# Optimization experiments

Hardware: AMD Instinct MI355X
Metric: run time of the kernel (lower is better)

## Reference

```python
import jax, jax.numpy as jnp
import numpy as np

N_NODES = 50000
N_EDGES = 200000
N_GRAPHS = 2048
EMB = 300
N_LAYERS = 5
BN_EPS = 1e-5


def setup_inputs() -> dict:
    key = jax.random.key(0)
    ks = jax.random.split(key, 16)
    s = 0.02
    d = {}
    d["atomic_number"] = jax.random.randint(ks[0], (N_NODES,), 0, 120)
    d["chirality_type"] = jax.random.randint(ks[1], (N_NODES,), 0, 3)
    d["bond_type"] = jax.random.randint(ks[2], (N_EDGES,), 0, 6)
    d["bond_direction_type"] = jax.random.randint(ks[3], (N_EDGES,), 0, 3)
    d["src"] = jax.random.randint(ks[4], (N_EDGES,), 0, N_NODES)
    d["dst"] = jax.random.randint(ks[5], (N_EDGES,), 0, N_NODES)
    d["graph_ids"] = jnp.sort(jax.random.randint(ks[6], (N_NODES,), 0, N_GRAPHS))
    d["num_graphs"] = N_GRAPHS
    d["node_emb0"] = jax.random.normal(ks[7], (120, EMB), jnp.float32) * s
    d["node_emb1"] = jax.random.normal(ks[8], (3, EMB), jnp.float32) * s
    d["edge_emb0"] = jax.random.normal(ks[9], (N_LAYERS, 6, EMB), jnp.float32) * s
    d["edge_emb1"] = jax.random.normal(ks[10], (N_LAYERS, 3, EMB), jnp.float32) * s
    d["W1"] = jax.random.normal(ks[11], (N_LAYERS, EMB, 2 * EMB), jnp.float32) * s
    d["b1"] = jnp.zeros((N_LAYERS, 2 * EMB), jnp.float32)
    d["W2"] = jax.random.normal(ks[12], (N_LAYERS, 2 * EMB, EMB), jnp.float32) * s
    d["b2"] = jnp.zeros((N_LAYERS, EMB), jnp.float32)
    d["bn_gamma"] = jnp.ones((N_LAYERS, EMB), jnp.float32)
    d["bn_beta"] = jnp.zeros((N_LAYERS, EMB), jnp.float32)
    d["bn_mean"] = jax.random.normal(ks[13], (N_LAYERS, EMB), jnp.float32) * s
    d["bn_var"] = jax.random.uniform(ks[14], (N_LAYERS, EMB), jnp.float32, 0.5, 1.5)
    return d


def gin_node_feats(atomic_number, chirality_type, bond_type, bond_direction_type,
                   src, dst, node_emb0, node_emb1, edge_emb0, edge_emb1,
                   W1, b1, W2, b2, bn_gamma, bn_beta, bn_mean, bn_var):
    n = atomic_number.shape[0]
    h = node_emb0[atomic_number] + node_emb1[chirality_type]  # [N, EMB]
    feats = [h]
    for l in range(N_LAYERS):
        # u_add_e message: src node feat + per-layer categorical edge embedding
        e = edge_emb0[l][bond_type] + edge_emb1[l][bond_direction_type]  # [E, EMB]
        m = feats[l][src] + e
        agg = jax.ops.segment_sum(m, dst, num_segments=n)  # sum aggregation at dst
        x = jax.nn.relu(agg @ W1[l] + b1[l]) @ W2[l] + b2[l]  # GIN MLP 300->600->300
        # BatchNorm1d in eval mode (running stats)
        x = (x - bn_mean[l]) * jax.lax.rsqrt(bn_var[l] + BN_EPS) * bn_gamma[l] + bn_beta[l]
        if l < N_LAYERS - 1:
            x = jax.nn.relu(x)  # activation on all but last layer
        feats.append(x)  # dropout is identity in eval mode
    return jnp.concatenate(feats, axis=1)  # JK='concat' -> [N, 6*EMB]


def reference(atomic_number, chirality_type, bond_type, bond_direction_type,
              src, dst, graph_ids, num_graphs,
              node_emb0, node_emb1, edge_emb0, edge_emb1,
              W1, b1, W2, b2, bn_gamma, bn_beta, bn_mean, bn_var):
    nf = gin_node_feats(atomic_number, chirality_type, bond_type, bond_direction_type,
                        src, dst, node_emb0, node_emb1, edge_emb0, edge_emb1,
                        W1, b1, W2, b2, bn_gamma, bn_beta, bn_mean, bn_var)
    sums = jax.ops.segment_sum(nf, graph_ids, num_segments=num_graphs)  # SumPooling
    counts = jax.ops.segment_sum(jnp.ones((nf.shape[0], 1), nf.dtype), graph_ids,
                                 num_segments=num_graphs)
    avg = sums / jnp.maximum(counts, 1.0)  # AvgPooling
    return jnp.concatenate([avg, sums], axis=1)  # [G, 2*6*EMB]
```

## Files before the change

kernel.cpp:

```cpp
#include <hip/hip_runtime.h>

#define EMB 300
#define HID 600
#define NL 5
#define BN_EPS 1e-5f

#define FS 320
#define HS 640
#define NPW 8
#define KS1 10
#define KS2 20

typedef __attribute__((ext_vector_type(8))) short short8;
typedef __attribute__((ext_vector_type(4))) float f32x4;
typedef __attribute__((ext_vector_type(4))) unsigned short us4;

__device__ __forceinline__ unsigned short f2bf(float x) {
    unsigned u = __float_as_uint(x);
    unsigned r = (u + 0x7FFFu + ((u >> 16) & 1u)) >> 16;
    return (unsigned short)r;
}
__device__ __forceinline__ float bf2f(unsigned short h) {
    return __uint_as_float(((unsigned)h) << 16);
}

#define GLDS16(gsrc, ldst)                                                     \
    __builtin_amdgcn_global_load_lds(                                          \
        (const __attribute__((address_space(1))) unsigned int*)(gsrc),         \
        (__attribute__((address_space(3))) unsigned int*)(ldst), 16, 0, 0)

__global__ void k_init_h0(const int* __restrict__ an, const int* __restrict__ ch,
                          const float* __restrict__ ne0, const float* __restrict__ ne1,
                          unsigned short* __restrict__ Fb, int n) {
    int t = blockIdx.x * blockDim.x + threadIdx.x;
    int i = t / (FS / 4), f4 = t - i * (FS / 4);
    if (i >= n) return;
    int f = f4 * 4;
    us4 h = {0, 0, 0, 0};
    if (f < EMB) {
        const float4 a = *(const float4*)(ne0 + (size_t)an[i] * EMB + f);
        const float4 b = *(const float4*)(ne1 + (size_t)ch[i] * EMB + f);
        h[0] = f2bf(a.x + b.x); h[1] = f2bf(a.y + b.y);
        h[2] = f2bf(a.z + b.z); h[3] = f2bf(a.w + b.w);
    }
    *(us4*)(Fb + (size_t)i * FS + f) = h;
}

__global__ void k_hist(const int* __restrict__ dst, const int* __restrict__ bt,
                       const int* __restrict__ bd, int* __restrict__ deg,
                       int* __restrict__ cnt9, int e) {
    int t = blockIdx.x * blockDim.x + threadIdx.x;
    if (t >= e) return;
    int d = dst[t];
    atomicAdd(&deg[d], 1);
    atomicAdd(&cnt9[d * 9 + bt[t]], 1);
    atomicAdd(&cnt9[d * 9 + 6 + bd[t]], 1);
}

__global__ __launch_bounds__(256)
void k_scan_blk(const int* __restrict__ deg, int* __restrict__ incl,
                int* __restrict__ part, int n) {
    int tid = threadIdx.x;
    int base = blockIdx.x * 1024 + tid * 4;
    int v0 = (base + 0 < n) ? deg[base + 0] : 0;
    int v1 = (base + 1 < n) ? deg[base + 1] : 0;
    int v2 = (base + 2 < n) ? deg[base + 2] : 0;
    int v3 = (base + 3 < n) ? deg[base + 3] : 0;
    int ts = v0 + v1 + v2 + v3;
    int lane = tid & 63, w = tid >> 6;
    int x = ts;
#pragma unroll
    for (int off = 1; off < 64; off <<= 1) {
        int y = __shfl_up(x, off);
        if (lane >= off) x += y;
    }
    __shared__ int ws[4];
    if (lane == 63) ws[w] = x;
    __syncthreads();
    int woff = 0;
    for (int i = 0; i < w; ++i) woff += ws[i];
    int r = woff + x - ts;
    r += v0; if (base + 0 < n) incl[base + 0] = r;
    r += v1; if (base + 1 < n) incl[base + 1] = r;
    r += v2; if (base + 2 < n) incl[base + 2] = r;
    r += v3; if (base + 3 < n) incl[base + 3] = r;
    if (tid == 255) part[blockIdx.x] = woff + x;
}

__global__ __launch_bounds__(1024)
void k_scan_part(int* __restrict__ part, int nb) {
    int tid = threadIdx.x;
    int v = (tid < nb) ? part[tid] : 0;
    int lane = tid & 63, w = tid >> 6;
    int x = v;
#pragma unroll
    for (int off = 1; off < 64; off <<= 1) {
        int y = __shfl_up(x, off);
        if (lane >= off) x += y;
    }
    __shared__ int ws[16];
    if (lane == 63) ws[w] = x;
    __syncthreads();
    int woff = 0;
    for (int i = 0; i < w; ++i) woff += ws[i];
    if (tid < nb) part[tid] = woff + x - v;
}

__global__ void k_scan_add(const int* __restrict__ incl, const int* __restrict__ part,
                           const int* __restrict__ deg, int* __restrict__ roff,
                           int* __restrict__ curs, int n) {
    int i = blockIdx.x * blockDim.x + threadIdx.x;
    if (i >= n) return;
    int inc = incl[i] + part[i >> 10];
    roff[i + 1] = inc;
    curs[i] = inc - deg[i];
    if (i == 0) roff[0] = 0;
}

__global__ void k_scatter(const int* __restrict__ dst, const int* __restrict__ src,
                          int* __restrict__ cursor, int* __restrict__ srcs, int e) {
    int t = blockIdx.x * blockDim.x + threadIdx.x;
    if (t < e) { int p = atomicAdd(&cursor[dst[t]], 1); srcs[p] = src[t]; }
}

__global__ void k_gbound(const int* __restrict__ gids, int* __restrict__ gstart,
                         int n, int G) {
    int i = blockIdx.x * blockDim.x + threadIdx.x;
    if (i >= n) return;
    int g = gids[i];
    int gp = (i == 0) ? -1 : gids[i - 1];
    for (int q = gp + 1; q <= g; ++q) gstart[q] = i;
    if (i == n - 1)
        for (int q = g + 1; q <= G; ++q) gstart[q] = n;
}

__global__ void k_prep_w1p(const float* __restrict__ W1, unsigned short* __restrict__ W1P,
                           int total) {
    int t = blockIdx.x * blockDim.x + threadIdx.x;
    if (t >= total) return;
    int lane = t & 63;
    int r = t >> 6;
    int ks = r % KS1; r /= KS1;
    int nf = r % 40;
    int l = r / 40;
    int n = nf * 16 + (lane & 15);
    int kb = ks * 32 + (lane >> 4) * 8;
    unsigned short v[8];
#pragma unroll
    for (int e = 0; e < 8; ++e) {
        int k = kb + e;
        v[e] = (n < HID && k < EMB) ? f2bf(W1[(size_t)l * EMB * HID + (size_t)k * HID + n]) : 0;
    }
    *(short8*)(W1P + (size_t)t * 8) = *(short8*)v;
}

__global__ void k_prep_w2p(const float* __restrict__ W2, unsigned short* __restrict__ W2P,
                           int total) {
    int t = blockIdx.x * blockDim.x + threadIdx.x;
    if (t >= total) return;
    int lane = t & 63;
    int r = t >> 6;
    int ks = r % KS2; r /= KS2;
    int nf = r % 20;
    int l = r / 20;
    int n = nf * 16 + (lane & 15);
    int kb = ks * 32 + (lane >> 4) * 8;
    unsigned short v[8];
#pragma unroll
    for (int e = 0; e < 8; ++e) {
        int k = kb + e;
        v[e] = (n < EMB && k < HID) ? f2bf(W2[(size_t)l * HID * EMB + (size_t)k * EMB + n]) : 0;
    }
    *(short8*)(W2P + (size_t)t * 8) = *(short8*)v;
}

__global__ void k_prep_params(const float* __restrict__ b1, const float* __restrict__ b2,
                              const float* __restrict__ g, const float* __restrict__ be,
                              const float* __restrict__ mu, const float* __restrict__ va,
                              float* __restrict__ b1p, float* __restrict__ scp,
                              float* __restrict__ shp, int total) {
    int t = blockIdx.x * blockDim.x + threadIdx.x;
    if (t >= total) return;
    int n = t % HS, l = t / HS;
    b1p[t] = (n < HID) ? b1[l * HID + n] : 0.f;
    if (n < FS) {
        float sc = 0.f, sh = 0.f;
        if (n < EMB) {
            sc = g[l * EMB + n] * rsqrtf(va[l * EMB + n] + BN_EPS);
            sh = be[l * EMB + n] + (b2[l * EMB + n] - mu[l * EMB + n]) * sc;
        }
        scp[l * FS + n] = sc;
        shp[l * FS + n] = sh;
    }
}

__global__ __launch_bounds__(256)
void k_aggregate(const unsigned short* __restrict__ fb,
                 const float* __restrict__ e0, const float* __restrict__ e1,
                 const int* __restrict__ roff, const int* __restrict__ srcs,
                 const int* __restrict__ cnt9,
                 unsigned short* __restrict__ agg, int n) {
    const int v0 = (blockIdx.x * 4 + (threadIdx.x >> 6)) * NPW;
    if (v0 >= n) return;
    const int lane = threadIdx.x & 63;
    const int nv = min(NPW, n - v0);

    int rv = 0;
    {
        int idx = v0 + lane;
        if (lane <= NPW && idx <= n) rv = roff[idx];
    }
    const int base = __shfl(rv, 0);
    const int total = __shfl(rv, nv) - base;

    const int n9 = n * 9;
    const int base9 = v0 * 9;
    int c0 = (base9 + lane < n9) ? cnt9[base9 + lane] : 0;
    int c1 = (lane < 8 && base9 + 64 + lane < n9) ? cnt9[base9 + 64 + lane] : 0;

    int c = 0;
    int chunk = 0;
    auto nextIdx = [&]() -> int {
        if ((c & 63) == 0)
            chunk = (c + lane < total) ? srcs[base + c + lane] : 0;
        int r = __shfl(chunk, c & 63);
        ++c;
        return r;
    };

#pragma unroll
    for (int i = 0; i < NPW; ++i) {
        if (i < nv) {
            const int di = __shfl(rv, i + 1) - __shfl(rv, i);
            float aA[4] = {0.f, 0.f, 0.f, 0.f};
            float aB[4] = {0.f, 0.f, 0.f, 0.f};
            int k = 0;
            for (; k + 4 <= di; k += 4) {
                int i0 = nextIdx(), i1 = nextIdx(), i2 = nextIdx(), i3 = nextIdx();
                const us4* r0 = (const us4*)(fb + (size_t)i0 * FS);
                const us4* r1 = (const us4*)(fb + (size_t)i1 * FS);
                const us4* r2 = (const us4*)(fb + (size_t)i2 * FS);
                const us4* r3 = (const us4*)(fb + (size_t)i3 * FS);
                us4 x0 = r0[lane], x1 = r1[lane], x2 = r2[lane], x3 = r3[lane];
                us4 y0 = {}, y1 = {}, y2 = {}, y3 = {};
                if (lane < 11) { y0 = r0[64 + lane]; y1 = r1[64 + lane];
                                 y2 = r2[64 + lane]; y3 = r3[64 + lane]; }
#pragma unroll
                for (int q = 0; q < 4; ++q)
                    aA[q] += (bf2f(x0[q]) + bf2f(x1[q])) + (bf2f(x2[q]) + bf2f(x3[q]));
                if (lane < 11) {
#pragma unroll
                    for (int q = 0; q < 4; ++q)
                        aB[q] += (bf2f(y0[q]) + bf2f(y1[q])) + (bf2f(y2[q]) + bf2f(y3[q]));
                }
            }
            for (; k < di; ++k) {
                int i0 = nextIdx();
                const us4* r0 = (const us4*)(fb + (size_t)i0 * FS);
                us4 x0 = r0[lane];
#pragma unroll
                for (int q = 0; q < 4; ++q) aA[q] += bf2f(x0[q]);
                if (lane < 11) {
                    us4 y0 = r0[64 + lane];
#pragma unroll
                    for (int q = 0; q < 4; ++q) aB[q] += bf2f(y0[q]);
                }
            }
#pragma unroll
            for (int t = 0; t < 9; ++t) {
                const int pos = i * 9 + t;
                int cv = __shfl(pos < 64 ? c0 : c1, pos & 63);
                if (cv) {
                    float fc = (float)cv;
                    const float* row = (t < 6) ? (e0 + t * EMB) : (e1 + (t - 6) * EMB);
                    f32x4 ea = *(const f32x4*)(row + 4 * lane);
#pragma unroll
                    for (int q = 0; q < 4; ++q) aA[q] += fc * ea[q];
                    if (lane < 11) {
                        f32x4 eb = *(const f32x4*)(row + 256 + 4 * lane);
#pragma unroll
                        for (int q = 0; q < 4; ++q) aB[q] += fc * eb[q];
                    }
                }
            }
            us4* ar = (us4*)(agg + (size_t)(v0 + i) * FS);
            us4 h;
#pragma unroll
            for (int q = 0; q < 4; ++q) h[q] = f2bf(aA[q]);
            ar[lane] = h;
            if (lane < 11) {
                us4 hb;
#pragma unroll
                for (int q = 0; q < 4; ++q) hb[q] = f2bf(aB[q]);
                ar[64 + lane] = hb;
            }
        }
    }
}

template <int EPI>
__global__ __launch_bounds__(512)
void k_mlp(const unsigned short* __restrict__ A,
           const unsigned short* __restrict__ W1P,
           const unsigned short* __restrict__ W2P,
           const float* __restrict__ b1p,
           const float* __restrict__ scp, const float* __restrict__ shp,
           unsigned short* __restrict__ Cout) {
    __shared__ unsigned short Ash[64 * 320];
    __shared__ unsigned short Hsh[64 * 640];
    const int tid = threadIdx.x;
    const int lane = tid & 63, wid = tid >> 6;
    const int lr = lane & 15, lk = lane >> 4, rgrp = lk * 4;
    const size_t m0s = (size_t)blockIdx.x * 64;

#pragma unroll
    for (int cch = 0; cch < 5; ++cch) {
        const int sbase = wid * 5120 + cch * 1024;
        const int s = sbase + lane * 16;
        const int row = s / 640;
        const int u = s ^ ((row & 7) << 4);
        GLDS16((const char*)A + m0s * 640 + u, (char*)Ash + sbase);
    }
    asm volatile("s_waitcnt vmcnt(0)" ::: "memory");
    __syncthreads();

    {
        f32x4 acc1[5][4] = {};
        short8 bw[5], bn_[5];
#pragma unroll
        for (int i = 0; i < 5; ++i)
            bw[i] = *(const short8*)(W1P + (((size_t)(wid * 5 + i) * KS1 + 0) * 64 + lane) * 8);
        for (int ks = 0; ks < KS1; ++ks) {
            if (ks + 1 < KS1) {
#pragma unroll
                for (int i = 0; i < 5; ++i)
                    bn_[i] = *(const short8*)(W1P + (((size_t)(wid * 5 + i) * KS1 + ks + 1) * 64 + lane) * 8);
            }
            short8 a[4];
#pragma unroll
            for (int j = 0; j < 4; ++j) {
                const int row = j * 16 + lr;
                const int o = (row * 640 + ks * 64 + lk * 16) ^ ((lr & 7) << 4);
                a[j] = *(const short8*)((const char*)Ash + o);
            }
#pragma unroll
            for (int i = 0; i < 5; ++i)
#pragma unroll
                for (int j = 0; j < 4; ++j)
                    acc1[i][j] = __builtin_amdgcn_mfma_f32_16x16x32_bf16(bw[i], a[j], acc1[i][j], 0, 0, 0);
#pragma unroll
            for (int i = 0; i < 5; ++i) bw[i] = bn_[i];
        }
#pragma unroll
        for (int i = 0; i < 5; ++i) {
            const int n0 = wid * 80 + i * 16 + rgrp;
            const f32x4 q0 = *(const f32x4*)&b1p[n0];
#pragma unroll
            for (int j = 0; j < 4; ++j) {
                const int m = j * 16 + lr;
                us4 h;
#pragma unroll
                for (int p = 0; p < 4; ++p)
                    h[p] = f2bf(fmaxf(acc1[i][j][p] + q0[p], 0.f));
                const int o = (m * 1280 + n0 * 2) ^ ((lr & 7) << 4);
                *(us4*)((char*)Hsh + o) = h;
            }
        }
    }
    __syncthreads();

    {
        const int wm2 = wid >> 2, wn2 = wid & 3;
        f32x4 acc2[5][2] = {};
        short8 cw[5], cn_[5];
#pragma unroll
        for (int i = 0; i < 5; ++i)
            cw[i] = *(const short8*)(W2P + (((size_t)(wn2 * 5 + i) * KS2 + 0) * 64 + lane) * 8);
        for (int ks = 0; ks < KS2; ++ks) {
            if (ks + 1 < KS2) {
#pragma unroll
                for (int i = 0; i < 5; ++i)
                    cn_[i] = *(const short8*)(W2P + (((size_t)(wn2 * 5 + i) * KS2 + ks + 1) * 64 + lane) * 8);
            }
            short8 a[2];
#pragma unroll
            for (int j = 0; j < 2; ++j) {
                const int row = wm2 * 32 + j * 16 + lr;
                const int o = (row * 1280 + ks * 64 + lk * 16) ^ ((lr & 7) << 4);
                a[j] = *(const short8*)((const char*)Hsh + o);
            }
#pragma unroll
            for (int i = 0; i < 5; ++i)
#pragma unroll
                for (int j = 0; j < 2; ++j)
                    acc2[i][j] = __builtin_amdgcn_mfma_f32_16x16x32_bf16(cw[i], a[j], acc2[i][j], 0, 0, 0);
#pragma unroll
            for (int i = 0; i < 5; ++i) cw[i] = cn_[i];
        }
#pragma unroll
        for (int i = 0; i < 5; ++i) {
            const int n0 = wn2 * 80 + i * 16 + rgrp;
            const f32x4 q0 = *(const f32x4*)&scp[n0];
            const f32x4 q1 = *(const f32x4*)&shp[n0];
#pragma unroll
            for (int j = 0; j < 2; ++j) {
                const size_t m = m0s + (size_t)(wm2 * 32 + j * 16 + lr);
                us4 h;
#pragma unroll
                for (int p = 0; p < 4; ++p) {
                    float x = acc2[i][j][p] * q0[p] + q1[p];
                    if (EPI == 1) x = fmaxf(x, 0.f);
                    h[p] = f2bf(x);
                }
                *(us4*)(Cout + m * FS + n0) = h;
            }
        }
    }
}

__global__ __launch_bounds__(256)
void k_pool(const unsigned short* __restrict__ feats, const int* __restrict__ gstart,
            float* __restrict__ out, int l) {
    const int g = blockIdx.x;
    const int tid = threadIdx.x;
    const int w = tid >> 6, lane = tid & 63;
    const int s = gstart[g], e = gstart[g + 1];
    float aA[4] = {0.f, 0.f, 0.f, 0.f};
    float aB[4] = {0.f, 0.f, 0.f, 0.f};
    int v = s + w;
    for (; v + 4 < e; v += 8) {
        const us4* r0 = (const us4*)(feats + (size_t)v * FS);
        const us4* r1 = (const us4*)(feats + (size_t)(v + 4) * FS);
        us4 x0 = r0[lane], x1 = r1[lane];
        us4 y0 = {}, y1 = {};
        if (lane < 11) { y0 = r0[64 + lane]; y1 = r1[64 + lane]; }
#pragma unroll
        for (int q = 0; q < 4; ++q) aA[q] += bf2f(x0[q]) + bf2f(x1[q]);
        if (lane < 11) {
#pragma unroll
            for (int q = 0; q < 4; ++q) aB[q] += bf2f(y0[q]) + bf2f(y1[q]);
        }
    }
    if (v < e) {
        const us4* r0 = (const us4*)(feats + (size_t)v * FS);
        us4 x0 = r0[lane];
#pragma unroll
        for (int q = 0; q < 4; ++q) aA[q] += bf2f(x0[q]);
        if (lane < 11) {
            us4 y0 = r0[64 + lane];
#pragma unroll
            for (int q = 0; q < 4; ++q) aB[q] += bf2f(y0[q]);
        }
    }
    __shared__ f32x4 smA[4][64];
    __shared__ f32x4 smB[4][16];
    f32x4 xa;
#pragma unroll
    for (int q = 0; q < 4; ++q) xa[q] = aA[q];
    smA[w][lane] = xa;
    if (lane < 16) {
        f32x4 xb;
#pragma unroll
        for (int q = 0; q < 4; ++q) xb[q] = aB[q];
        smB[w][lane] = xb;
    }
    __syncthreads();
    if (w == 0) {
        f32x4 t = smA[0][lane] + smA[1][lane] + smA[2][lane] + smA[3][lane];
        float inv = 1.0f / fmaxf((float)(e - s), 1.0f);
        float* oavg = out + (size_t)g * (12 * EMB) + l * EMB;
        float* osum = oavg + 6 * EMB;
        *(f32x4*)(oavg + 4 * lane) = t * inv;
        *(f32x4*)(osum + 4 * lane) = t;
        if (lane < 11) {
            f32x4 tb = smB[0][lane] + smB[1][lane] + smB[2][lane] + smB[3][lane];
            *(f32x4*)(oavg + 256 + 4 * lane) = tb * inv;
            *(f32x4*)(osum + 256 + 4 * lane) = tb;
        }
    }
}

extern "C" void kernel_launch(void* const* d_in, const int* in_sizes, int n_in,
                              void* d_out, int out_size, void* d_ws, size_t ws_size,
                              hipStream_t stream) {
    const int*   an  = (const int*)d_in[0];
    const int*   ch  = (const int*)d_in[1];
    const int*   bt  = (const int*)d_in[2];
    const int*   bd  = (const int*)d_in[3];
    const int*   src = (const int*)d_in[4];
    const int*   dst = (const int*)d_in[5];
    const int*   gid = (const int*)d_in[6];
    const float* ne0 = (const float*)d_in[8];
    const float* ne1 = (const float*)d_in[9];
    const float* ee0 = (const float*)d_in[10];
    const float* ee1 = (const float*)d_in[11];
    const float* W1  = (const float*)d_in[12];
    const float* b1  = (const float*)d_in[13];
    const float* W2  = (const float*)d_in[14];
    const float* b2  = (const float*)d_in[15];
    const float* bng = (const float*)d_in[16];
    const float* bnb = (const float*)d_in[17];
    const float* bnm = (const float*)d_in[18];
    const float* bnv = (const float*)d_in[19];

    const int N = in_sizes[0];
    const int E = in_sizes[2];
    const int G = out_size / (12 * EMB);
    const int M_pad = ((N + 63) / 64) * 64;
    const int MT = M_pad / 64;
    const int nb = (N + 1023) / 1024;

    char* ws = (char*)d_ws;
    size_t off = 0;
    auto alloc = [&](size_t bytes) -> void* {
        void* p = (void*)(ws + off);
        off += (bytes + 255) & ~(size_t)255;
        return p;
    };
    unsigned short* Fb0  = (unsigned short*)alloc((size_t)M_pad * FS * 2);
    unsigned short* Fb1  = (unsigned short*)alloc((size_t)M_pad * FS * 2);
    unsigned short* A1   = (unsigned short*)alloc((size_t)M_pad * FS * 2);
    unsigned short* W1P  = (unsigned short*)alloc((size_t)NL * 40 * KS1 * 64 * 8 * 2);
    unsigned short* W2P  = (unsigned short*)alloc((size_t)NL * 20 * KS2 * 64 * 8 * 2);
    float*          b1p  = (float*)alloc((size_t)NL * HS * 4);
    float*          scp  = (float*)alloc((size_t)NL * FS * 4);
    float*          shp  = (float*)alloc((size_t)NL * FS * 4);
    int*            deg  = (int*)alloc((size_t)N * 4);
    int*            roff = (int*)alloc(((size_t)N + 1) * 4);
    int*            curs = (int*)alloc((size_t)N * 4);
    int*            srcs = (int*)alloc((size_t)E * 4);
    int*            cnt9 = (int*)alloc((size_t)N * 9 * 4);
    int*            incl = (int*)alloc((size_t)N * 4);
    int*            part = (int*)alloc((size_t)1024 * 4);
    int*            gst  = (int*)alloc(((size_t)G + 1) * 4);

    {
        int t1 = NL * 40 * KS1 * 64;
        k_prep_w1p<<<(t1 + 255) / 256, 256, 0, stream>>>(W1, W1P, t1);
        int t2 = NL * 20 * KS2 * 64;
        k_prep_w2p<<<(t2 + 255) / 256, 256, 0, stream>>>(W2, W2P, t2);
        int t3 = NL * HS;
        k_prep_params<<<(t3 + 255) / 256, 256, 0, stream>>>(b1, b2, bng, bnb, bnm, bnv,
                                                            b1p, scp, shp, t3);
    }

    {
        int tt = N * (FS / 4);
        k_init_h0<<<(tt + 255) / 256, 256, 0, stream>>>(an, ch, ne0, ne1, Fb0, N);
    }

    hipMemsetAsync(deg, 0, (size_t)N * 4, stream);
    hipMemsetAsync(cnt9, 0, (size_t)N * 9 * 4, stream);
    k_hist<<<(E + 255) / 256, 256, 0, stream>>>(dst, bt, bd, deg, cnt9, E);
    k_scan_blk<<<nb, 256, 0, stream>>>(deg, incl, part, N);
    k_scan_part<<<1, 1024, 0, stream>>>(part, nb);
    k_scan_add<<<(N + 255) / 256, 256, 0, stream>>>(incl, part, deg, roff, curs, N);
    k_scatter<<<(E + 255) / 256, 256, 0, stream>>>(dst, src, curs, srcs, E);
    k_gbound<<<(N + 255) / 256, 256, 0, stream>>>(gid, gst, N, G);

    const int aggBlocks = (N + 4 * NPW - 1) / (4 * NPW);

    unsigned short* Fbc = Fb0;
    unsigned short* Fbo = Fb1;
    for (int l = 0; l < NL; ++l) {
        k_pool<<<G, 256, 0, stream>>>(Fbc, gst, (float*)d_out, l);
        k_aggregate<<<aggBlocks, 256, 0, stream>>>(Fbc,
                                                   ee0 + (size_t)l * 6 * EMB,
                                                   ee1 + (size_t)l * 3 * EMB,
                                                   roff, srcs, cnt9, A1, N);
        const unsigned short* W1Pl = W1P + (size_t)l * 40 * KS1 * 64 * 8;
        const unsigned short* W2Pl = W2P + (size_t)l * 20 * KS2 * 64 * 8;
        if (l < NL - 1)
            k_mlp<1><<<MT, 512, 0, stream>>>(A1, W1Pl, W2Pl,
                                             b1p + (size_t)l * HS,
                                             scp + (size_t)l * FS, shp + (size_t)l * FS,
                                             Fbo);
        else
            k_mlp<2><<<MT, 512, 0, stream>>>(A1, W1Pl, W2Pl,
                                             b1p + (size_t)l * HS,
                                             scp + (size_t)l * FS, shp + (size_t)l * FS,
                                             Fbo);
        unsigned short* t = Fbc; Fbc = Fbo; Fbo = t;
    }
    k_pool<<<G, 256, 0, stream>>>(Fbc, gst, (float*)d_out, NL);
}
```

Baseline: 755.3 us.

## Load MLP inputs directly from global, drop A staging in LDS, retile GEMM1

The fused MLP kernel no longer stages the 64-row input tile in LDS through global_load_lds. Each wave now reads its A fragments straight from global memory, and GEMM1 is retiled into 2x4 waves over two column halves. The weight prefetch double-buffering is removed, MFMA blocks are wrapped in s_setprio, and launch bounds request 4 blocks per CU. Cutting LDS use is meant to raise occupancy and drop a barrier, in exchange for redundant global loads of A across waves and no explicit latency hiding for weight loads.

```diff
diff --git a/kernel.cpp b/kernel.cpp
--- a/kernel.cpp
+++ b/kernel.cpp
@@ -23,11 +23,6 @@
 __device__ __forceinline__ float bf2f(unsigned short h) {
     return __uint_as_float(((unsigned)h) << 16);
 }
-
-#define GLDS16(gsrc, ldst)                                                     \
-    __builtin_amdgcn_global_load_lds(                                          \
-        (const __attribute__((address_space(1))) unsigned int*)(gsrc),         \
-        (__attribute__((address_space(3))) unsigned int*)(ldst), 16, 0, 0)
 
 __global__ void k_init_h0(const int* __restrict__ an, const int* __restrict__ ch,
                           const float* __restrict__ ne0, const float* __restrict__ ne1,
@@ -299,120 +294,109 @@
 }
 
 template <int EPI>
-__global__ __launch_bounds__(512)
+__global__ __launch_bounds__(512, 4)
 void k_mlp(const unsigned short* __restrict__ A,
            const unsigned short* __restrict__ W1P,
            const unsigned short* __restrict__ W2P,
            const float* __restrict__ b1p,
            const float* __restrict__ scp, const float* __restrict__ shp,
            unsigned short* __restrict__ Cout) {
-    __shared__ unsigned short Ash[64 * 320];
     __shared__ unsigned short Hsh[64 * 640];
     const int tid = threadIdx.x;
     const int lane = tid & 63, wid = tid >> 6;
+    const int wm = wid >> 2, wn = wid & 3;
     const int lr = lane & 15, lk = lane >> 4, rgrp = lk * 4;
-    const size_t m0s = (size_t)blockIdx.x * 64;
-
-#pragma unroll
-    for (int cch = 0; cch < 5; ++cch) {
-        const int sbase = wid * 5120 + cch * 1024;
-        const int s = sbase + lane * 16;
-        const int row = s / 640;
-        const int u = s ^ ((row & 7) << 4);
-        GLDS16((const char*)A + m0s * 640 + u, (char*)Ash + sbase);
-    }
-    asm volatile("s_waitcnt vmcnt(0)" ::: "memory");
+    const size_t m0 = (size_t)blockIdx.x * 64;
+
+    const unsigned short* a0p = A + (m0 + (size_t)(wm * 32 + lr)) * FS + lk * 8;
+    const unsigned short* a1p = a0p + (size_t)16 * FS;
+
+#pragma unroll
+    for (int h = 0; h < 2; ++h) {
+        f32x4 acc1[5][2] = {};
+        const unsigned short* wp = W1P + ((size_t)(h * 20 + wn * 5) * KS1 * 64 + lane) * 8;
+        for (int ks = 0; ks < KS1; ++ks) {
+            short8 a0 = *(const short8*)(a0p + ks * 32);
+            short8 a1 = *(const short8*)(a1p + ks * 32);
+            short8 w0 = *(const short8*)(wp + ((size_t)(0 * KS1 + ks) * 64) * 8);
+            short8 w1 = *(const short8*)(wp + ((size_t)(1 * KS1 + ks) * 64) * 8);
+            short8 w2 = *(const short8*)(wp + ((size_t)(2 * KS1 + ks) * 64) * 8);
+            short8 w3 = *(const short8*)(wp + ((size_t)(3 * KS1 + ks) * 64) * 8);
+            short8 w4 = *(const short8*)(wp + ((size_t)(4 * KS1 + ks) * 64) * 8);
+            __builtin_amdgcn_s_setprio(1);
+            acc1[0][0] = __builtin_amdgcn_mfma_f32_16x16x32_bf16(w0, a0, acc1[0][0], 0, 0, 0);
+            acc1[0][1] = __builtin_amdgcn_mfma_f32_16x16x32_bf16(w0, a1, acc1[0][1], 0, 0, 0);
+            acc1[1][0] = __builtin_amdgcn_mfma_f32_16x16x32_bf16(w1, a0, acc1[1][0], 0, 0, 0);
+            acc1[1][1] = __builtin_amdgcn_mfma_f32_16x16x32_bf16(w1, a1, acc1[1][1], 0, 0, 0);
+            acc1[2][0] = __builtin_amdgcn_mfma_f32_16x16x32_bf16(w2, a0, acc1[2][0], 0, 0, 0);
+            acc1[2][1] = __builtin_amdgcn_mfma_f32_16x16x32_bf16(w2, a1, acc1[2][1], 0, 0, 0);
+            acc1[3][0] = __builtin_amdgcn_mfma_f32_16x16x32_bf16(w3, a0, acc1[3][0], 0, 0, 0);
+            acc1[3][1] = __builtin_amdgcn_mfma_f32_16x16x32_bf16(w3, a1, acc1[3][1], 0, 0, 0);
+            acc1[4][0] = __builtin_amdgcn_mfma_f32_16x16x32_bf16(w4, a0, acc1[4][0], 0, 0, 0);
+            acc1[4][1] = __builtin_amdgcn_mfma_f32_16x16x32_bf16(w4, a1, acc1[4][1], 0, 0, 0);
+            __builtin_amdgcn_s_setprio(0);
+        }
+#pragma unroll
+        for (int i = 0; i < 5; ++i) {
+            const int n0 = h * 320 + wn * 80 + i * 16 + rgrp;
+            const f32x4 q0 = *(const f32x4*)&b1p[n0];
+#pragma unroll
+            for (int j = 0; j < 2; ++j) {
+                const int m = wm * 32 + j * 16 + lr;
+                us4 hh;
+#pragma unroll
+                for (int p = 0; p < 4; ++p)
+                    hh[p] = f2bf(fmaxf(acc1[i][j][p] + q0[p], 0.f));
+                const int o = (m * 1280 + n0 * 2) ^ ((lr & 7) << 4);
+                *(us4*)((char*)Hsh + o) = hh;
+            }
+        }
+    }
     __syncthreads();
 
     {
-        f32x4 acc1[5][4] = {};
-        short8 bw[5], bn_[5];
-#pragma unroll
-        for (int i = 0; i < 5; ++i)
-            bw[i] = *(const short8*)(W1P + (((size_t)(wid * 5 + i) * KS1 + 0) * 64 + lane) * 8);
-        for (int ks = 0; ks < KS1; ++ks) {
-            if (ks + 1 < KS1) {
-#pragma unroll
-                for (int i = 0; i < 5; ++i)
-                    bn_[i] = *(const short8*)(W1P + (((size_t)(wid * 5 + i) * KS1 + ks + 1) * 64 + lane) * 8);
-            }
-            short8 a[4];
-#pragma unroll
-            for (int j = 0; j < 4; ++j) {
-                const int row = j * 16 + lr;
-                const int o = (row * 640 + ks * 64 + lk * 16) ^ ((lr & 7) << 4);
-                a[j] = *(const short8*)((const char*)Ash + o);
-            }
-#pragma unroll
-            for (int i = 0; i < 5; ++i)
-#pragma unroll
-                for (int j = 0; j < 4; ++j)
-                    acc1[i][j] = __builtin_amdgcn_mfma_f32_16x16x32_bf16(bw[i], a[j], acc1[i][j], 0, 0, 0);
-#pragma unroll
-            for (int i = 0; i < 5; ++i) bw[i] = bn_[i];
+        f32x4 acc2[5][2] = {};
+        const unsigned short* wp = W2P + ((size_t)(wn * 5) * KS2 * 64 + lane) * 8;
+        const int row0 = wm * 32 + lr;
+        for (int ks = 0; ks < KS2; ++ks) {
+            const int o0 = (row0 * 1280 + ks * 64 + lk * 16) ^ ((lr & 7) << 4);
+            const int o1 = ((row0 + 16) * 1280 + ks * 64 + lk * 16) ^ ((lr & 7) << 4);
+            short8 h0 = *(const short8*)((const char*)Hsh + o0);
+            short8 h1 = *(const short8*)((const char*)Hsh + o1);
+            short8 w0 = *(const short8*)(wp + ((size_t)(0 * KS2 + ks) * 64) * 8);
+            short8 w1 = *(const short8*)(wp + ((size_t)(1 * KS2 + ks) * 64) * 8);
+            short8 w2 = *(const short8*)(wp + ((size_t)(2 * KS2 + ks) * 64) * 8);
+            short8 w3 = *(const short8*)(wp + ((size_t)(3 * KS2 + ks) * 64) * 8);
+            short8 w4 = *(const short8*)(wp + ((size_t)(4 * KS2 + ks) * 64) * 8);
+            __builtin_amdgcn_s_setprio(1);
+            acc2[0][0] = __builtin_amdgcn_mfma_f32_16x16x32_bf16(w0, h0, acc2[0][0], 0, 0, 0);
+            acc2[0][1] = __builtin_amdgcn_mfma_f32_16x16x32_bf16(w0, h1, acc2[0][1], 0, 0, 0);
+            acc2[1][0] = __builtin_amdgcn_mfma_f32_16x16x32_bf16(w1, h0, acc2[1][0], 0, 0, 0);
+            acc2[1][1] = __builtin_amdgcn_mfma_f32_16x16x32_bf16(w1, h1, acc2[1][1], 0, 0, 0);
+            acc2[2][0] = __builtin_amdgcn_mfma_f32_16x16x32_bf16(w2, h0, acc2[2][0], 0, 0, 0);
+            acc2[2][1] = __builtin_amdgcn_mfma_f32_16x16x32_bf16(w2, h1, acc2[2][1], 0, 0, 0);
+            acc2[3][0] = __builtin_amdgcn_mfma_f32_16x16x32_bf16(w3, h0, acc2[3][0], 0, 0, 0);
+            acc2[3][1] = __builtin_amdgcn_mfma_f32_16x16x32_bf16(w3, h1, acc2[3][1], 0, 0, 0);
+            acc2[4][0] = __builtin_amdgcn_mfma_f32_16x16x32_bf16(w4, h0, acc2[4][0], 0, 0, 0);
+            acc2[4][1] = __builtin_amdgcn_mfma_f32_16x16x32_bf16(w4, h1, acc2[4][1], 0, 0, 0);
+            __builtin_amdgcn_s_setprio(0);
         }
 #pragma unroll
         for (int i = 0; i < 5; ++i) {
-            const int n0 = wid * 80 + i * 16 + rgrp;
-            const f32x4 q0 = *(const f32x4*)&b1p[n0];
-#pragma unroll
-            for (int j = 0; j < 4; ++j) {
-                const int m = j * 16 + lr;
-                us4 h;
-#pragma unroll
-                for (int p = 0; p < 4; ++p)
-                    h[p] = f2bf(fmaxf(acc1[i][j][p] + q0[p], 0.f));
-                const int o = (m * 1280 + n0 * 2) ^ ((lr & 7) << 4);
-                *(us4*)((char*)Hsh + o) = h;
-            }
-        }
-    }
-    __syncthreads();
-
-    {
-        const int wm2 = wid >> 2, wn2 = wid & 3;
-        f32x4 acc2[5][2] = {};
-        short8 cw[5], cn_[5];
-#pragma unroll
-        for (int i = 0; i < 5; ++i)
-            cw[i] = *(const short8*)(W2P + (((size_t)(wn2 * 5 + i) * KS2 + 0) * 64 + lane) * 8);
-        for (int ks = 0; ks < KS2; ++ks) {
-            if (ks + 1 < KS2) {
-#pragma unroll
-                for (int i = 0; i < 5; ++i)
-                    cn_[i] = *(const short8*)(W2P + (((size_t)(wn2 * 5 + i) * KS2 + ks + 1) * 64 + lane) * 8);
-            }
-            short8 a[2];
-#pragma unroll
-            for (int j = 0; j < 2; ++j) {
-                const int row = wm2 * 32 + j * 16 + lr;
-                const int o = (row * 1280 + ks * 64 + lk * 16) ^ ((lr & 7) << 4);
-                a[j] = *(const short8*)((const char*)Hsh + o);
-            }
-#pragma unroll
-            for (int i = 0; i < 5; ++i)
-#pragma unroll
-                for (int j = 0; j < 2; ++j)
-                    acc2[i][j] = __builtin_amdgcn_mfma_f32_16x16x32_bf16(cw[i], a[j], acc2[i][j], 0, 0, 0);
-#pragma unroll
-            for (int i = 0; i < 5; ++i) cw[i] = cn_[i];
-        }
-#pragma unroll
-        for (int i = 0; i < 5; ++i) {
-            const int n0 = wn2 * 80 + i * 16 + rgrp;
+            const int n0 = wn * 80 + i * 16 + rgrp;
             const f32x4 q0 = *(const f32x4*)&scp[n0];
             const f32x4 q1 = *(const f32x4*)&shp[n0];
 #pragma unroll
             for (int j = 0; j < 2; ++j) {
-                const size_t m = m0s + (size_t)(wm2 * 32 + j * 16 + lr);
-                us4 h;
+                const size_t m = m0 + (size_t)(wm * 32 + j * 16 + lr);
+                us4 hh;
 #pragma unroll
                 for (int p = 0; p < 4; ++p) {
                     float x = acc2[i][j][p] * q0[p] + q1[p];
                     if (EPI == 1) x = fmaxf(x, 0.f);
-                    h[p] = f2bf(x);
+                    hh[p] = f2bf(x);
                 }
-                *(us4*)(Cout + m * FS + n0) = h;
+                *(us4*)(Cout + m * FS + n0) = hh;
             }
         }
     }
```

After: 846.1 us. 1.12x slower.

## Software-pipeline MLP weight loads with inline asm double buffering and setprio

Applied to the files above, without the earlier changes.

Rewrites both GEMM phases of the fused MLP kernel as a hand-unrolled double-buffered pipeline. Each step issues raw global_load_dwordx4 for the next two k-steps of weights, waits with explicit vmcnt counts and sched barriers, and wraps each MFMA burst in s_setprio. It also issues the first W1 and W2 weight loads before the preceding barriers, and sets launch bounds to ask for two blocks per CU. The aim is to hide weight-fetch latency behind MFMA work, at the cost of much higher register pressure and a risk of spills or lower occupancy.

```diff
diff --git a/kernel.cpp b/kernel.cpp
--- a/kernel.cpp
+++ b/kernel.cpp
@@ -28,6 +28,24 @@
     __builtin_amdgcn_global_load_lds(                                          \
         (const __attribute__((address_space(1))) unsigned int*)(gsrc),         \
         (__attribute__((address_space(3))) unsigned int*)(ldst), 16, 0, 0)
+
+#define GLOAD8(dst, ptr)                                                       \
+    asm volatile("global_load_dwordx4 %0, %1, off" : "=v"(dst) : "v"(ptr))
+
+#define MFMA(d, w, a) d = __builtin_amdgcn_mfma_f32_16x16x32_bf16(w, a, d, 0, 0, 0)
+
+#define LSET(W, P, KS)                                                         \
+    GLOAD8(W##0, P[0] + (KS) * 512); GLOAD8(W##1, P[1] + (KS) * 512);          \
+    GLOAD8(W##2, P[2] + (KS) * 512); GLOAD8(W##3, P[3] + (KS) * 512);          \
+    GLOAD8(W##4, P[4] + (KS) * 512);                                           \
+    GLOAD8(W##5, P[0] + ((KS) + 1) * 512); GLOAD8(W##6, P[1] + ((KS) + 1) * 512); \
+    GLOAD8(W##7, P[2] + ((KS) + 1) * 512); GLOAD8(W##8, P[3] + ((KS) + 1) * 512); \
+    GLOAD8(W##9, P[4] + ((KS) + 1) * 512);
+
+#define WAITK do { asm volatile("s_waitcnt vmcnt(10)" ::: "memory");           \
+                   __builtin_amdgcn_sched_barrier(0); } while (0)
+#define WAIT0 do { asm volatile("s_waitcnt vmcnt(0)" ::: "memory");            \
+                   __builtin_amdgcn_sched_barrier(0); } while (0)
 
 __global__ void k_init_h0(const int* __restrict__ an, const int* __restrict__ ch,
                           const float* __restrict__ ne0, const float* __restrict__ ne1,
@@ -299,7 +317,7 @@
 }
 
 template <int EPI>
-__global__ __launch_bounds__(512)
+__global__ __launch_bounds__(512, 2)
 void k_mlp(const unsigned short* __restrict__ A,
            const unsigned short* __restrict__ W1P,
            const unsigned short* __restrict__ W2P,
@@ -312,6 +330,7 @@
     const int lane = tid & 63, wid = tid >> 6;
     const int lr = lane & 15, lk = lane >> 4, rgrp = lk * 4;
     const size_t m0s = (size_t)blockIdx.x * 64;
+    const int swz = (lr & 7) << 4;
 
 #pragma unroll
     for (int cch = 0; cch < 5; ++cch) {
@@ -321,82 +340,116 @@
         const int u = s ^ ((row & 7) << 4);
         GLDS16((const char*)A + m0s * 640 + u, (char*)Ash + sbase);
     }
+
+    const unsigned short* p1[5];
+#pragma unroll
+    for (int i = 0; i < 5; ++i)
+        p1[i] = W1P + (((size_t)(wid * 5 + i) * KS1) * 64 + lane) * 8;
+    short8 wA0, wA1, wA2, wA3, wA4, wA5, wA6, wA7, wA8, wA9;
+    short8 wB0, wB1, wB2, wB3, wB4, wB5, wB6, wB7, wB8, wB9;
+    LSET(wA, p1, 0);
+
     asm volatile("s_waitcnt vmcnt(0)" ::: "memory");
+    __builtin_amdgcn_sched_barrier(0);
     __syncthreads();
 
+    f32x4 acc1[5][4] = {};
+
+#define G1_PH(W, KS)                                                           \
+    do {                                                                       \
+        short8 a[8];                                                           \
+        _Pragma("unroll")                                                      \
+        for (int j = 0; j < 4; ++j) {                                          \
+            const int o0 = ((j * 16 + lr) * 640 + (KS) * 64 + lk * 16) ^ swz;  \
+            const int o1 = ((j * 16 + lr) * 640 + ((KS) + 1) * 64 + lk * 16) ^ swz; \
+            a[j] = *(const short8*)((const char*)Ash + o0);                    \
+            a[4 + j] = *(const short8*)((const char*)Ash + o1);                \
+        }                                                                      \
+        __builtin_amdgcn_s_setprio(1);                                         \
+        _Pragma("unroll")                                                      \
+        for (int j = 0; j < 4; ++j) {                                          \
+            MFMA(acc1[0][j], W##0, a[j]); MFMA(acc1[1][j], W##1, a[j]);        \
+            MFMA(acc1[2][j], W##2, a[j]); MFMA(acc1[3][j], W##3, a[j]);        \
+            MFMA(acc1[4][j], W##4, a[j]);                                      \
+        }                                                                      \
+        _Pragma("unroll")                                                      \
+        for (int j = 0; j < 4; ++j) {                                          \
+            MFMA(acc1[0][j], W##5, a[4 + j]); MFMA(acc1[1][j], W##6, a[4 + j]);\
+            MFMA(acc1[2][j], W##7, a[4 + j]); MFMA(acc1[3][j], W##8, a[4 + j]);\
+            MFMA(acc1[4][j], W##9, a[4 + j]);                                  \
+        }                                                                      \
+        __builtin_amdgcn_s_setprio(0);                                         \
+    } while (0)
+
+    LSET(wB, p1, 2); WAITK; G1_PH(wA, 0);
+    LSET(wA, p1, 4); WAITK; G1_PH(wB, 2);
+    LSET(wB, p1, 6); WAITK; G1_PH(wA, 4);
+    LSET(wA, p1, 8); WAITK; G1_PH(wB, 6);
+    WAIT0;                  G1_PH(wA, 8);
+
+#pragma unroll
+    for (int i = 0; i < 5; ++i) {
+        const int n0 = wid * 80 + i * 16 + rgrp;
+        const f32x4 q0 = *(const f32x4*)&b1p[n0];
+#pragma unroll
+        for (int j = 0; j < 4; ++j) {
+            const int m = j * 16 + lr;
+            us4 h;
+#pragma unroll
+            for (int p = 0; p < 4; ++p)
+                h[p] = f2bf(fmaxf(acc1[i][j][p] + q0[p], 0.f));
+            const int o = (m * 1280 + n0 * 2) ^ swz;
+            *(us4*)((char*)Hsh + o) = h;
+        }
+    }
+
+    const int wm2 = wid >> 2, wn2 = wid & 3;
+    const unsigned short* p2[5];
+#pragma unroll
+    for (int i = 0; i < 5; ++i)
+        p2[i] = W2P + (((size_t)(wn2 * 5 + i) * KS2) * 64 + lane) * 8;
+    LSET(wA, p2, 0);
+    __syncthreads();
+
     {
-        f32x4 acc1[5][4] = {};
-        short8 bw[5], bn_[5];
-#pragma unroll
-        for (int i = 0; i < 5; ++i)
-            bw[i] = *(const short8*)(W1P + (((size_t)(wid * 5 + i) * KS1 + 0) * 64 + lane) * 8);
-        for (int ks = 0; ks < KS1; ++ks) {
-            if (ks + 1 < KS1) {
-#pragma unroll
-                for (int i = 0; i < 5; ++i)
-                    bn_[i] = *(const short8*)(W1P + (((size_t)(wid * 5 + i) * KS1 + ks + 1) * 64 + lane) * 8);
-            }
-            short8 a[4];
-#pragma unroll
-            for (int j = 0; j < 4; ++j) {
-                const int row = j * 16 + lr;
-                const int o = (row * 640 + ks * 64 + lk * 16) ^ ((lr & 7) << 4);
-                a[j] = *(const short8*)((const char*)Ash + o);
-            }
-#pragma unroll
-            for (int i = 0; i < 5; ++i)
-#pragma unroll
-                for (int j = 0; j < 4; ++j)
-                    acc1[i][j] = __builtin_amdgcn_mfma_f32_16x16x32_bf16(bw[i], a[j], acc1[i][j], 0, 0, 0);
-#pragma unroll
-            for (int i = 0; i < 5; ++i) bw[i] = bn_[i];
-        }
-#pragma unroll
-        for (int i = 0; i < 5; ++i) {
-            const int n0 = wid * 80 + i * 16 + rgrp;
-            const f32x4 q0 = *(const f32x4*)&b1p[n0];
-#pragma unroll
-            for (int j = 0; j < 4; ++j) {
-                const int m = j * 16 + lr;
-                us4 h;
-#pragma unroll
-                for (int p = 0; p < 4; ++p)
-                    h[p] = f2bf(fmaxf(acc1[i][j][p] + q0[p], 0.f));
-                const int o = (m * 1280 + n0 * 2) ^ ((lr & 7) << 4);
-                *(us4*)((char*)Hsh + o) = h;
-            }
-        }
-    }
-    __syncthreads();
-
-    {
-        const int wm2 = wid >> 2, wn2 = wid & 3;
+        const int r0 = wm2 * 32 + lr;
         f32x4 acc2[5][2] = {};
-        short8 cw[5], cn_[5];
-#pragma unroll
-        for (int i = 0; i < 5; ++i)
-            cw[i] = *(const short8*)(W2P + (((size_t)(wn2 * 5 + i) * KS2 + 0) * 64 + lane) * 8);
-        for (int ks = 0; ks < KS2; ++ks) {
-            if (ks + 1 < KS2) {
-#pragma unroll
-                for (int i = 0; i < 5; ++i)
-                    cn_[i] = *(const short8*)(W2P + (((size_t)(wn2 * 5 + i) * KS2 + ks + 1) * 64 + lane) * 8);
-            }
-            short8 a[2];
-#pragma unroll
-            for (int j = 0; j < 2; ++j) {
-                const int row = wm2 * 32 + j * 16 + lr;
-                const int o = (row * 1280 + ks * 64 + lk * 16) ^ ((lr & 7) << 4);
-                a[j] = *(const short8*)((const char*)Hsh + o);
-            }
-#pragma unroll
-            for (int i = 0; i < 5; ++i)
-#pragma unroll
-                for (int j = 0; j < 2; ++j)
-                    acc2[i][j] = __builtin_amdgcn_mfma_f32_16x16x32_bf16(cw[i], a[j], acc2[i][j], 0, 0, 0);
-#pragma unroll
-            for (int i = 0; i < 5; ++i) cw[i] = cn_[i];
-        }
+
+#define G2_PH(W, KS)                                                           \
+    do {                                                                       \
+        const int o0 = (r0 * 1280 + (KS) * 64 + lk * 16) ^ swz;                \
+        const int o1 = ((r0 + 16) * 1280 + (KS) * 64 + lk * 16) ^ swz;         \
+        const int o2 = (r0 * 1280 + ((KS) + 1) * 64 + lk * 16) ^ swz;          \
+        const int o3 = ((r0 + 16) * 1280 + ((KS) + 1) * 64 + lk * 16) ^ swz;   \
+        short8 h0 = *(const short8*)((const char*)Hsh + o0);                   \
+        short8 h1 = *(const short8*)((const char*)Hsh + o1);                   \
+        short8 h2 = *(const short8*)((const char*)Hsh + o2);                   \
+        short8 h3 = *(const short8*)((const char*)Hsh + o3);                   \
+        __builtin_amdgcn_s_setprio(1);                                         \
+        MFMA(acc2[0][0], W##0, h0); MFMA(acc2[0][1], W##0, h1);                \
+        MFMA(acc2[1][0], W##1, h0); MFMA(acc2[1][1], W##1, h1);                \
+        MFMA(acc2[2][0], W##2, h0); MFMA(acc2[2][1], W##2, h1);                \
+        MFMA(acc2[3][0], W##3, h0); MFMA(acc2[3][1], W##3, h1);                \
+        MFMA(acc2[4][0], W##4, h0); MFMA(acc2[4][1], W##4, h1);                \
+        MFMA(acc2[0][0], W##5, h2); MFMA(acc2[0][1], W##5, h3);                \
+        MFMA(acc2[1][0], W##6, h2); MFMA(acc2[1][1], W##6, h3);                \
+        MFMA(acc2[2][0], W##7, h2); MFMA(acc2[2][1], W##7, h3);                \
+        MFMA(acc2[3][0], W##8, h2); MFMA(acc2[3][1], W##8, h3);                \
+        MFMA(acc2[4][0], W##9, h2); MFMA(acc2[4][1], W##9, h3);                \
+        __builtin_amdgcn_s_setprio(0);                                         \
+    } while (0)
+
+        LSET(wB, p2, 2);  WAITK; G2_PH(wA, 0);
+        LSET(wA, p2, 4);  WAITK; G2_PH(wB, 2);
+        LSET(wB, p2, 6);  WAITK; G2_PH(wA, 4);
+        LSET(wA, p2, 8);  WAITK; G2_PH(wB, 6);
+        LSET(wB, p2, 10); WAITK; G2_PH(wA, 8);
+        LSET(wA, p2, 12); WAITK; G2_PH(wB, 10);
+        LSET(wB, p2, 14); WAITK; G2_PH(wA, 12);
+        LSET(wA, p2, 16); WAITK; G2_PH(wB, 14);
+        LSET(wB, p2, 18); WAITK; G2_PH(wA, 16);
+        WAIT0;                   G2_PH(wB, 18);
+
 #pragma unroll
         for (int i = 0; i < 5; ++i) {
             const int n0 = wn2 * 80 + i * 16 + rgrp;
```

Result: faster. 698.4 us (-7.5%).
